# Performance work log

Hardware: AMD Instinct MI355X
Metric: run time of the kernel (lower is better)

## Reference

```python
import jax, jax.numpy as jnp
import numpy as np

DIM = 384
DIM_HEAD = 32
HEADS = DIM // DIM_HEAD  # 12
WIN = 8
DIM_FF = 1536
FUSED = DIM + DIM + DIM_FF  # 2304


def setup_inputs() -> dict:
    key = jax.random.key(0)
    ks = jax.random.split(key, 8)
    B, H, W = 16, 64, 64
    x = jax.random.normal(ks[0], (B, DIM, H, W), dtype=jnp.float32)
    s = lambda fan_in: 1.0 / np.sqrt(fan_in)
    w_fused = jax.random.normal(ks[1], (FUSED, DIM), dtype=jnp.float32) * s(DIM)
    w_gate = jax.random.normal(ks[2], (HEADS, DIM), dtype=jnp.float32) * s(DIM)
    b_gate = jnp.full((HEADS,), 0.5, dtype=jnp.float32)  # init_constant_(0.5)
    w_attn_out = jax.random.normal(ks[3], (DIM, DIM), dtype=jnp.float32) * s(DIM)
    w_ff_out = jax.random.normal(ks[4], (DIM, DIM_FF), dtype=jnp.float32) * s(DIM_FF)
    # StarReLU learnable scalars (metaformer defaults)
    sr_scale = jnp.asarray(0.8944, dtype=jnp.float32)
    sr_bias = jnp.asarray(-0.4472, dtype=jnp.float32)
    return {"x": x, "w_fused": w_fused, "w_gate": w_gate, "b_gate": b_gate,
            "w_attn_out": w_attn_out, "w_ff_out": w_ff_out,
            "sr_scale": sr_scale, "sr_bias": sr_bias}


def reference(x, w_fused, w_gate, b_gate, w_attn_out, w_ff_out, sr_scale, sr_bias):
    B, C, H, W = x.shape
    p = WIN
    gh, gw = H // p, W // p
    n = p * p
    # b c (h p1) (w p2) -> (b h w) (p1 p2) c
    xw = x.reshape(B, C, gh, p, gw, p).transpose(0, 2, 4, 3, 5, 1).reshape(B * gh * gw, n, C)
    fused = jnp.einsum('bnc,fc->bnf', xw, w_fused)  # [Bw, n, 2304]
    q, kv, x_ff = jnp.split(fused, [DIM, 2 * DIM], axis=-1)
    # b n (h d) -> b h n d
    q = q.reshape(-1, n, HEADS, DIM_HEAD).transpose(0, 2, 1, 3)
    kv = kv.reshape(-1, n, HEADS, DIM_HEAD).transpose(0, 2, 1, 3)
    scale = 1.0 / np.sqrt(DIM_HEAD)
    scores = jnp.einsum('bhnd,bhmd->bhnm', q, kv) * scale
    attn = jax.nn.softmax(scores, axis=-1)
    x_attn = jnp.einsum('bhnm,bhmd->bhnd', attn, kv)  # kv is both key and value
    gate = jnp.einsum('bnc,hc->bnh', xw, w_gate) + b_gate  # [Bw, n, heads]
    x_attn = x_attn * jax.nn.sigmoid(gate.transpose(0, 2, 1)[..., None])
    x_attn = x_attn.transpose(0, 2, 1, 3).reshape(-1, n, DIM)
    ff = sr_scale * jnp.square(jax.nn.relu(x_ff)) + sr_bias  # StarReLU
    out = jnp.einsum('bnc,oc->bno', x_attn, w_attn_out) + jnp.einsum('bnf,of->bno', ff, w_ff_out)
    # (b h w) (p1 p2) c -> b c (h p1) (w p2)
    out = out.reshape(B, gh, gw, p, p, C).transpose(0, 5, 1, 3, 2, 4).reshape(B, C, H, W)
    return out
```

## Files before the change

### kernel.cpp

```cpp
#include <hip/hip_runtime.h>
#include <hip/hip_bf16.h>

typedef __bf16 bf16x8 __attribute__((ext_vector_type(8), may_alias));
typedef float f32x4 __attribute__((ext_vector_type(4), may_alias));
typedef unsigned short ushort_a __attribute__((may_alias));
typedef unsigned int uint_a __attribute__((may_alias));
typedef unsigned short us8 __attribute__((ext_vector_type(8), may_alias));

#define MFMA(a, b, c) __builtin_amdgcn_mfma_f32_16x16x32_bf16(a, b, c, 0, 0, 0)

__device__ __forceinline__ unsigned short f2bf(float f) {
  return __builtin_bit_cast(unsigned short, (__bf16)f);
}
__device__ __forceinline__ float bf2f(unsigned short u) {
  unsigned v = ((unsigned)u) << 16;
  return __builtin_bit_cast(float, v);
}

__device__ __forceinline__ void kbar() {
  __builtin_amdgcn_sched_barrier(0);
  asm volatile("s_waitcnt lgkmcnt(0)" ::: "memory");
  __builtin_amdgcn_sched_barrier(0);
  __builtin_amdgcn_s_barrier();
  __builtin_amdgcn_sched_barrier(0);
}

#define GLOAD(G, L)                                                          \
  __builtin_amdgcn_global_load_lds(                                          \
      (const __attribute__((address_space(1))) unsigned int*)(G),            \
      (__attribute__((address_space(3))) unsigned int*)(L), 16, 0, 0)

#define OFF_WG 884736
#define OFF_WAO 933888
#define OFF_WFO 1081344
#define OFF_XG 1671168
#define OFF_FUSED 26836992
#define OFF_GATE 177831936

__global__ __launch_bounds__(256) void prep_weights(
    const float* __restrict__ wf, const float* __restrict__ wg,
    const float* __restrict__ wao, const float* __restrict__ wfo,
    unsigned short* __restrict__ ws) {
  int i = blockIdx.x * 256 + threadIdx.x;
  if (i < 884736) { ws[i] = f2bf(wf[i]); return; }
  int j = i - 884736;
  if (j < 49152) { ws[i] = f2bf(j < 4608 ? wg[j] : 0.0f); return; }
  j -= 49152;
  if (j < 147456) { ws[i] = f2bf(wao[j]); return; }
  j -= 147456;
  if (j < 589824) ws[i] = f2bf(wfo[j]);
}

__global__ __launch_bounds__(256) void k0_gather(const float* __restrict__ x,
                                                 unsigned short* __restrict__ xg) {
  __shared__ __align__(16) char As[49152];
  int tid = threadIdx.x, wi = blockIdx.x;
  int b = wi >> 6, ghi = (wi >> 3) & 7, gwi = wi & 7;
  const float* xb = x + (size_t)b * 1572864 + (ghi * 8) * 64 + gwi * 8;
  for (int it = 0; it < 12; ++it) {
    int idx = it * 256 + tid;
    int c = idx % 384, p1 = idx / 384;
    const float* src = xb + (size_t)c * 4096 + p1 * 64;
    float4 v0 = *(const float4*)src, v1 = *(const float4*)(src + 4);
    float f[8] = {v0.x, v0.y, v0.z, v0.w, v1.x, v1.y, v1.z, v1.w};
#pragma unroll
    for (int jj = 0; jj < 8; ++jj) {
      int row = p1 * 8 + jj;
      int byte = (row * 768 + c * 2) ^ ((row & 7) << 4);
      *(ushort_a*)(As + byte) = f2bf(f[jj]);
    }
  }
  __syncthreads();
  unsigned short* og = xg + (size_t)wi * 24576;
#pragma unroll
  for (int it = 0; it < 12; ++it) {
    int idx = it * 256 + tid;
    int row = idx / 48, c = idx % 48;
    int byte = (row * 768 + c * 16) ^ ((row & 7) << 4);
    *(us8*)(og + (size_t)row * 384 + c * 8) = *(us8*)(As + byte);
  }
}

__global__ __launch_bounds__(512, 4) void k1_gemm(unsigned short* __restrict__ ws,
                                                  const float* __restrict__ srs,
                                                  const float* __restrict__ srb) {
  __shared__ __align__(16) char sm[65536];
  const int tid = threadIdx.x, lane = tid & 63, wave = tid >> 6;
  const int l15 = lane & 15, l4 = lane >> 4;
  const int wr = wave & 3, wc = wave >> 2;
  const int bid = blockIdx.x;
  const int swz = (bid & 7) * 1216 + (bid >> 3);
  const int mb = swz / 19, nb = swz - mb * 19;
  const unsigned short* Ab = ws + OFF_XG + (size_t)mb * 128 * 384;
  const unsigned short* Bb =
      (nb < 18) ? ws + (size_t)nb * 128 * 384 : ws + OFF_WG;
  const int srow = tid >> 3, sc = tid & 7;
  f32x4 of[2][4] = {};
  us8 sA0[2], sB0[2], sA1[2], sB1[2];

#define K1_LOAD(KS, SA, SB)                                                   \
  {                                                                           \
    _Pragma("unroll") for (int r2 = 0; r2 < 2; ++r2) {                        \
      int row = srow + 64 * r2;                                               \
      SA[r2] = *(const us8*)(Ab + (size_t)row * 384 + (KS)*64 + sc * 8);      \
      SB[r2] = *(const us8*)(Bb + (size_t)row * 384 + (KS)*64 + sc * 8);      \
    }                                                                         \
  }
#define K1_WRITE(BUF, SA, SB)                                                 \
  {                                                                           \
    _Pragma("unroll") for (int r2 = 0; r2 < 2; ++r2) {                        \
      int row = srow + 64 * r2;                                               \
      int byte = ((row * 128 + sc * 16) ^ ((row & 7) << 4)) + (BUF);          \
      *(us8*)(sm + byte) = SA[r2];                                            \
      *(us8*)(sm + 32768 + byte) = SB[r2];                                    \
    }                                                                         \
  }
#define K1_COMPUTE(BUF)                                                       \
  {                                                                           \
    _Pragma("unroll") for (int kk = 0; kk < 2; ++kk) {                        \
      bf16x8 af[2], bfr[4];                                                   \
      _Pragma("unroll") for (int mt = 0; mt < 2; ++mt) {                      \
        int row = wr * 32 + mt * 16 + l15;                                    \
        af[mt] = *(const bf16x8*)(sm + (BUF) +                                \
                 ((row * 128 + kk * 64 + l4 * 16) ^ ((row & 7) << 4)));       \
      }                                                                       \
      _Pragma("unroll") for (int nt = 0; nt < 4; ++nt) {                      \
        int row = wc * 64 + nt * 16 + l15;                                    \
        bfr[nt] = *(const bf16x8*)(sm + 32768 + (BUF) +                       \
                  ((row * 128 + kk * 64 + l4 * 16) ^ ((row & 7) << 4)));      \
      }                                                                       \
      _Pragma("unroll") for (int mt = 0; mt < 2; ++mt)                        \
      _Pragma("unroll") for (int nt = 0; nt < 4; ++nt)                        \
          of[mt][nt] = MFMA(af[mt], bfr[nt], of[mt][nt]);                     \
    }                                                                         \
  }

  K1_LOAD(0, sA0, sB0);
  K1_LOAD(1, sA1, sB1);
  K1_WRITE(0, sA0, sB0);
  __syncthreads();
#pragma unroll 1
  for (int kp = 0; kp < 3; ++kp) {
    int ks = kp * 2;
    if (ks + 2 < 6) K1_LOAD(ks + 2, sA0, sB0);
    K1_COMPUTE(0);
    K1_WRITE(16384, sA1, sB1);
    kbar();
    if (ks + 3 < 6) K1_LOAD(ks + 3, sA1, sB1);
    K1_COMPUTE(16384);
    if (ks + 2 < 6) K1_WRITE(0, sA0, sB0);
    kbar();
  }
  const float ssc = srs[0], sbi = srb[0];
  const bool ffreg = (nb >= 6) && (nb < 18);
#pragma unroll
  for (int mt = 0; mt < 2; ++mt)
#pragma unroll
    for (int nt = 0; nt < 4; ++nt)
#pragma unroll
      for (int rr = 0; rr < 4; ++rr) {
        int row = wr * 32 + mt * 16 + l4 * 4 + rr;
        int col = wc * 64 + nt * 16 + l15;
        float v = of[mt][nt][rr];
        if (ffreg) { v = fmaxf(v, 0.0f); v = ssc * v * v + sbi; }
        *(ushort_a*)(sm + ((row * 256 + col * 2) ^ ((row & 7) << 4))) = f2bf(v);
      }
  __syncthreads();
  if (nb < 18) {
    unsigned short* fo = ws + OFF_FUSED + (size_t)mb * 128 * 2304 + nb * 128;
#pragma unroll
    for (int r2 = 0; r2 < 4; ++r2) {
      int idx = r2 * 512 + tid;
      int row = idx >> 4, c = idx & 15;
      int byte = (row * 256 + c * 16) ^ ((row & 7) << 4);
      __builtin_nontemporal_store(*(us8*)(sm + byte),
                                  (us8*)(fo + (size_t)row * 2304 + c * 8));
    }
  } else {
    unsigned short* go = ws + OFF_GATE + (size_t)mb * 128 * 16;
#pragma unroll
    for (int r2 = 0; r2 < 4; ++r2) {
      int idx = r2 * 512 + tid;
      int row = idx >> 4, c = idx & 15;
      if (c < 2) {
        int byte = (row * 256 + c * 16) ^ ((row & 7) << 4);
        __builtin_nontemporal_store(*(us8*)(sm + byte),
                                    (us8*)(go + (size_t)row * 16 + c * 8));
      }
    }
  }
}

__global__ __launch_bounds__(256, 3) void k2_attn(unsigned short* __restrict__ ws,
                                                  const float* __restrict__ bgate) {
  __shared__ __align__(16) char sm[49152];
  const int tid = threadIdx.x, lane = tid & 63, wave = tid >> 6;
  const int l15 = lane & 15, l4 = lane >> 4;
  char* kvT = sm + wave * 12288;
  char* Pb = kvT + 4096;
  const int wi = blockIdx.x;
  const size_t T0 = (size_t)wi * 64;
  unsigned short* fused = ws + OFF_FUSED;
  const unsigned short* gb = ws + OFF_GATE;
  const f32x4 zz = {};
#pragma unroll 1
  for (int hi = 0; hi < 3; ++hi) {
    const int h = wave + hi * 4;
    bf16x8 akv[4], bq[4];
#pragma unroll
    for (int t = 0; t < 4; ++t) {
      akv[t] = *(const bf16x8*)(fused + (T0 + t * 16 + l15) * 2304 + 384 + h * 32 + l4 * 8);
      bq[t] = *(const bf16x8*)(fused + (T0 + t * 16 + l15) * 2304 + h * 32 + l4 * 8);
    }
    f32x4 sfT[4][4];
#pragma unroll
    for (int mt = 0; mt < 4; ++mt)
#pragma unroll
      for (int ni = 0; ni < 4; ++ni) sfT[mt][ni] = MFMA(akv[mt], bq[ni], zz);
#pragma unroll
    for (int mt = 0; mt < 4; ++mt) {
      us8 u = __builtin_bit_cast(us8, akv[mt]);
      int m = mt * 16 + l15;
#pragma unroll
      for (int j = 0; j < 8; ++j) {
        int d = l4 * 8 + j;
        *(ushort_a*)(kvT + ((d * 128 + m * 2) ^ ((d & 7) << 4))) = u[j];
      }
    }
#pragma unroll
    for (int ni = 0; ni < 4; ++ni) {
      float s[16];
#pragma unroll
      for (int mt = 0; mt < 4; ++mt)
#pragma unroll
        for (int rr = 0; rr < 4; ++rr)
          s[mt * 4 + rr] = sfT[mt][ni][rr] * 0.176776695f;
      float mx = s[0];
#pragma unroll
      for (int q2 = 1; q2 < 16; ++q2) mx = fmaxf(mx, s[q2]);
      mx = fmaxf(mx, __shfl_xor(mx, 16, 64));
      mx = fmaxf(mx, __shfl_xor(mx, 32, 64));
      float sum = 0.0f;
#pragma unroll
      for (int q2 = 0; q2 < 16; ++q2) {
        s[q2] = __expf(s[q2] - mx);
        sum += s[q2];
      }
      sum += __shfl_xor(sum, 16, 64);
      sum += __shfl_xor(sum, 32, 64);
      float rs = 1.0f / sum;
      int n = ni * 16 + l15;
      int rowb = n * 128, sw = (n & 7) << 4;
#pragma unroll
      for (int mt = 0; mt < 4; ++mt) {
        int m = mt * 16 + l4 * 4;
        unsigned p0 = (unsigned)f2bf(s[mt * 4 + 0] * rs) |
                      ((unsigned)f2bf(s[mt * 4 + 1] * rs) << 16);
        unsigned p1 = (unsigned)f2bf(s[mt * 4 + 2] * rs) |
                      ((unsigned)f2bf(s[mt * 4 + 3] * rs) << 16);
        *(uint_a*)(Pb + ((rowb + m * 2) ^ sw)) = p0;
        *(uint_a*)(Pb + ((rowb + (m + 2) * 2) ^ sw)) = p1;
      }
    }
    f32x4 xo[4][2] = {};
#pragma unroll
    for (int ks = 0; ks < 2; ++ks) {
      bf16x8 bv[2];
#pragma unroll
      for (int dt = 0; dt < 2; ++dt) {
        int d = dt * 16 + l15;
        bv[dt] = *(const bf16x8*)(kvT + ((d * 128 + ks * 64 + l4 * 16) ^ ((d & 7) << 4)));
      }
#pragma unroll
      for (int nt = 0; nt < 4; ++nt) {
        int n = nt * 16 + l15;
        bf16x8 ap = *(const bf16x8*)(Pb + ((n * 128 + ks * 64 + l4 * 16) ^ ((n & 7) << 4)));
        xo[nt][0] = MFMA(ap, bv[0], xo[nt][0]);
        xo[nt][1] = MFMA(ap, bv[1], xo[nt][1]);
      }
    }
    const float bgh = bgate[h];
#pragma unroll
    for (int nt = 0; nt < 4; ++nt)
#pragma unroll
      for (int rr = 0; rr < 4; ++rr) {
        int n = nt * 16 + l4 * 4 + rr;
        float gv = bf2f(gb[(T0 + n) * 16 + h]) + bgh;
        float sg = 1.0f / (1.0f + __expf(-gv));
#pragma unroll
        for (int dt = 0; dt < 2; ++dt)
          fused[(T0 + n) * 2304 + h * 32 + dt * 16 + l15] =
              f2bf(xo[nt][dt][rr] * sg);
      }
  }
}

__global__ __launch_bounds__(256, 2) void k3_gemm(const unsigned short* __restrict__ ws,
                                                  float* __restrict__ out) {
  __shared__ __align__(1024) char sm[65536];
  const int tid = threadIdx.x, lane = tid & 63, wave = tid >> 6;
  const int l15 = lane & 15, l4 = lane >> 4;
  const int wr = wave & 1, wc = wave >> 1;
  const int bid = blockIdx.x;
  const int swz = (bid & 7) * 192 + (bid >> 3);
  const int mb = swz / 3, nB = swz - mb * 3;
  const size_t T0 = (size_t)mb * 128;
  const unsigned short* fA = ws + OFF_FUSED + T0 * 2304;
  const unsigned short* wao = ws + OFF_WAO + (size_t)(nB * 128) * 384;
  const unsigned short* wfo = ws + OFF_WFO + (size_t)(nB * 128) * 1536;
  const int lr = lane >> 3, lc = (lane & 7) ^ lr;
  const int offA = lr * 2304 + lc * 8;
  const int offB384 = lr * 384 + lc * 8;
  const int offB1536 = lr * 1536 + lc * 8;
  f32x4 of[4][4] = {};

#define K3_STAGE(KS, BUF)                                                     \
  {                                                                           \
    const int ac_ = (KS) < 6 ? (KS)*64 : 768 + ((KS)-6) * 64;                 \
    _Pragma("unroll") for (int i = 0; i < 4; ++i) {                           \
      const int R = wave * 32 + i * 8;                                        \
      GLOAD(fA + (size_t)R * 2304 + ac_ + offA, sm + (BUF) + R * 128);        \
      if ((KS) < 6)                                                           \
        GLOAD(wao + (size_t)R * 384 + (KS)*64 + offB384,                      \
              sm + 32768 + (BUF) + R * 128);                                  \
      else                                                                    \
        GLOAD(wfo + (size_t)R * 1536 + ((KS)-6) * 64 + offB1536,              \
              sm + 32768 + (BUF) + R * 128);                                  \
    }                                                                         \
  }

  K3_STAGE(0, 0);
#pragma unroll 1
  for (int ks = 0; ks < 30; ++ks) {
    const int cur = (ks & 1) * 16384;
    if (ks + 1 < 30) K3_STAGE(ks + 1, 16384 - cur);
    __builtin_amdgcn_sched_barrier(0);
    if (ks + 1 < 30)
      asm volatile("s_waitcnt vmcnt(8)" ::: "memory");
    else
      asm volatile("s_waitcnt vmcnt(0)" ::: "memory");
    __builtin_amdgcn_sched_barrier(0);
    __builtin_amdgcn_s_barrier();
    __builtin_amdgcn_sched_barrier(0);
#pragma unroll
    for (int kk = 0; kk < 2; ++kk) {
      bf16x8 af[4], bfr[4];
#pragma unroll
      for (int mt = 0; mt < 4; ++mt) {
        int row = wr * 64 + mt * 16 + l15;
        af[mt] = *(const bf16x8*)(sm + cur +
                 ((row * 128 + kk * 64 + l4 * 16) ^ ((row & 7) << 4)));
      }
#pragma unroll
      for (int nt = 0; nt < 4; ++nt) {
        int row = wc * 64 + nt * 16 + l15;
        bfr[nt] = *(const bf16x8*)(sm + 32768 + cur +
                  ((row * 128 + kk * 64 + l4 * 16) ^ ((row & 7) << 4)));
      }
#pragma unroll
      for (int mt = 0; mt < 4; ++mt)
#pragma unroll
        for (int nt = 0; nt < 4; ++nt)
          of[mt][nt] = MFMA(af[mt], bfr[nt], of[mt][nt]);
    }
    kbar();
  }
#pragma unroll
  for (int mt = 0; mt < 4; ++mt) {
    int n0 = wr * 64 + mt * 16 + l4 * 4;
    int T = (int)T0 + n0;
    int wi = T >> 6, n = T & 63;
    int b = wi >> 6, ghi = (wi >> 3) & 7, gwi = wi & 7;
    float* ob = out + (size_t)b * 1572864 + (size_t)(ghi * 8 + (n >> 3)) * 64 +
                gwi * 8 + (n & 7);
#pragma unroll
    for (int nt = 0; nt < 4; ++nt) {
      int c = nB * 128 + wc * 64 + nt * 16 + l15;
      __builtin_nontemporal_store(of[mt][nt], (f32x4*)(ob + (size_t)c * 4096));
    }
  }
}

extern "C" void kernel_launch(void* const* d_in, const int* in_sizes, int n_in,
                              void* d_out, int out_size, void* d_ws, size_t ws_size,
                              hipStream_t stream) {
  const float* x = (const float*)d_in[0];
  const float* wf = (const float*)d_in[1];
  const float* wg = (const float*)d_in[2];
  const float* bg = (const float*)d_in[3];
  const float* wao = (const float*)d_in[4];
  const float* wfo = (const float*)d_in[5];
  const float* srs = (const float*)d_in[6];
  const float* srb = (const float*)d_in[7];
  unsigned short* ws = (unsigned short*)d_ws;

  prep_weights<<<6528, 256, 0, stream>>>(wf, wg, wao, wfo, ws);
  k0_gather<<<1024, 256, 0, stream>>>(x, ws + OFF_XG);
  k1_gemm<<<512 * 19, 512, 0, stream>>>(ws, srs, srb);
  k2_attn<<<1024, 256, 0, stream>>>(ws, bg);
  k3_gemm<<<512 * 3, 256, 0, stream>>>(ws, (float*)d_out);
}
```

Before: 474.4 us.

## Load k3 A operand directly into registers with triple-buffered prefetch, halve LDS

In the output GEMM kernel, the A tile (fused activations) is now loaded straight from global memory into MFMA register fragments, rotating through three register buffers two stages ahead. Only the B weight tile still goes through LDS, which halves shared memory per block and removes the LDS round-trip and ds_reads for A. The trade-off is higher VGPR pressure and uncoalesced per-lane 16-byte global loads with strided rows, which may lower occupancy or memory efficiency.

```diff
diff --git a/kernel.cpp b/kernel.cpp
--- a/kernel.cpp
+++ b/kernel.cpp
@@ -297,7 +297,7 @@
 
 __global__ __launch_bounds__(256, 2) void k3_gemm(const unsigned short* __restrict__ ws,
                                                   float* __restrict__ out) {
-  __shared__ __align__(1024) char sm[65536];
+  __shared__ __align__(1024) char sm[32768];
   const int tid = threadIdx.x, lane = tid & 63, wave = tid >> 6;
   const int l15 = lane & 15, l4 = lane >> 4;
   const int wr = wave & 1, wc = wave >> 1;
@@ -309,61 +309,72 @@
   const unsigned short* wao = ws + OFF_WAO + (size_t)(nB * 128) * 384;
   const unsigned short* wfo = ws + OFF_WFO + (size_t)(nB * 128) * 1536;
   const int lr = lane >> 3, lc = (lane & 7) ^ lr;
-  const int offA = lr * 2304 + lc * 8;
   const int offB384 = lr * 384 + lc * 8;
   const int offB1536 = lr * 1536 + lc * 8;
+  const unsigned short* Ar = fA + (size_t)(wr * 64 + l15) * 2304 + l4 * 8;
   f32x4 of[4][4] = {};
-
-#define K3_STAGE(KS, BUF)                                                     \
+  bf16x8 A0[8], A1[8], A2[8];
+
+#define K3_LOADA(KS, S)                                                       \
   {                                                                           \
     const int ac_ = (KS) < 6 ? (KS)*64 : 768 + ((KS)-6) * 64;                 \
+    _Pragma("unroll") for (int mt = 0; mt < 4; ++mt)                          \
+    _Pragma("unroll") for (int kk = 0; kk < 2; ++kk)                          \
+        S[mt * 2 + kk] =                                                      \
+            *(const bf16x8*)(Ar + (size_t)mt * 16 * 2304 + ac_ + kk * 32);    \
+  }
+#define K3_STAGEB(KS, BUF)                                                    \
+  {                                                                           \
     _Pragma("unroll") for (int i = 0; i < 4; ++i) {                           \
       const int R = wave * 32 + i * 8;                                        \
-      GLOAD(fA + (size_t)R * 2304 + ac_ + offA, sm + (BUF) + R * 128);        \
       if ((KS) < 6)                                                           \
-        GLOAD(wao + (size_t)R * 384 + (KS)*64 + offB384,                      \
-              sm + 32768 + (BUF) + R * 128);                                  \
+        GLOAD(wao + (size_t)R * 384 + (KS)*64 + offB384, sm + (BUF) + R * 128); \
       else                                                                    \
         GLOAD(wfo + (size_t)R * 1536 + ((KS)-6) * 64 + offB1536,              \
-              sm + 32768 + (BUF) + R * 128);                                  \
-    }                                                                         \
-  }
-
-  K3_STAGE(0, 0);
+              sm + (BUF) + R * 128);                                          \
+    }                                                                         \
+  }
+#define K3_COMPUTE(S, BUF)                                                    \
+  {                                                                           \
+    _Pragma("unroll") for (int kk = 0; kk < 2; ++kk) {                        \
+      bf16x8 bfr[4];                                                          \
+      _Pragma("unroll") for (int nt = 0; nt < 4; ++nt) {                      \
+        int row = wc * 64 + nt * 16 + l15;                                    \
+        bfr[nt] = *(const bf16x8*)(sm + (BUF) +                               \
+                  ((row * 128 + kk * 64 + l4 * 16) ^ ((row & 7) << 4)));      \
+      }                                                                       \
+      _Pragma("unroll") for (int mt = 0; mt < 4; ++mt)                        \
+      _Pragma("unroll") for (int nt = 0; nt < 4; ++nt)                        \
+          of[mt][nt] = MFMA(S[mt * 2 + kk], bfr[nt], of[mt][nt]);             \
+    }                                                                         \
+  }
+#define K3_PHASE(KS, USE, NEXT)                                               \
+  {                                                                           \
+    const int cur_ = ((KS)&1) * 16384;                                        \
+    if ((KS) + 1 < 30) K3_STAGEB((KS) + 1, 16384 - cur_);                     \
+    if ((KS) + 2 < 30) K3_LOADA((KS) + 2, NEXT);                              \
+    __builtin_amdgcn_sched_barrier(0);                                        \
+    if ((KS) < 29) {                                                          \
+      asm volatile("s_waitcnt vmcnt(12)" ::: "memory");                       \
+    } else {                                                                  \
+      asm volatile("s_waitcnt vmcnt(0)" ::: "memory");                        \
+    }                                                                         \
+    __builtin_amdgcn_sched_barrier(0);                                        \
+    __builtin_amdgcn_s_barrier();                                             \
+    __builtin_amdgcn_sched_barrier(0);                                        \
+    K3_COMPUTE(USE, cur_);                                                    \
+    kbar();                                                                   \
+  }
+
+  K3_LOADA(0, A0);
+  K3_LOADA(1, A1);
+  K3_STAGEB(0, 0);
 #pragma unroll 1
-  for (int ks = 0; ks < 30; ++ks) {
-    const int cur = (ks & 1) * 16384;
-    if (ks + 1 < 30) K3_STAGE(ks + 1, 16384 - cur);
-    __builtin_amdgcn_sched_barrier(0);
-    if (ks + 1 < 30)
-      asm volatile("s_waitcnt vmcnt(8)" ::: "memory");
-    else
-      asm volatile("s_waitcnt vmcnt(0)" ::: "memory");
-    __builtin_amdgcn_sched_barrier(0);
-    __builtin_amdgcn_s_barrier();
-    __builtin_amdgcn_sched_barrier(0);
-#pragma unroll
-    for (int kk = 0; kk < 2; ++kk) {
-      bf16x8 af[4], bfr[4];
-#pragma unroll
-      for (int mt = 0; mt < 4; ++mt) {
-        int row = wr * 64 + mt * 16 + l15;
-        af[mt] = *(const bf16x8*)(sm + cur +
-                 ((row * 128 + kk * 64 + l4 * 16) ^ ((row & 7) << 4)));
-      }
-#pragma unroll
-      for (int nt = 0; nt < 4; ++nt) {
-        int row = wc * 64 + nt * 16 + l15;
-        bfr[nt] = *(const bf16x8*)(sm + 32768 + cur +
-                  ((row * 128 + kk * 64 + l4 * 16) ^ ((row & 7) << 4)));
-      }
-#pragma unroll
-      for (int mt = 0; mt < 4; ++mt)
-#pragma unroll
-        for (int nt = 0; nt < 4; ++nt)
-          of[mt][nt] = MFMA(af[mt], bfr[nt], of[mt][nt]);
-    }
-    kbar();
+  for (int kp = 0; kp < 10; ++kp) {
+    const int ks = kp * 3;
+    K3_PHASE(ks, A0, A2);
+    K3_PHASE(ks + 1, A1, A0);
+    K3_PHASE(ks + 2, A2, A1);
   }
 #pragma unroll
   for (int mt = 0; mt < 4; ++mt) {
```

Result: slower. 611.5 us (+28.9%).
